# Optimization experiments

Hardware: AMD Instinct MI355X
Metric: run time of the kernel (lower is better)

Reference implementation:

```python
import jax, jax.numpy as jnp
import numpy as np

N_QUBITS = 6
N_LAYERS = 2
QSVT_DEGREE = 3
BATCH = 128
SEQ_LEN = 512
DIM = 2 ** N_QUBITS
# wire 0 is the most-significant bit in the statevector index (PennyLane convention)
_POP = np.array([bin(i).count('1') for i in range(DIM)], dtype=np.float32)
PHASE_SIGN = jnp.asarray(N_QUBITS - 2.0 * _POP)  # (DIM,): sum_w (1 - 2*bit_w)


def _rx(t):
    c = jnp.cos(0.5 * t).astype(jnp.complex64)
    s = (-1j * jnp.sin(0.5 * t)).astype(jnp.complex64)
    return jnp.stack([jnp.stack([c, s]), jnp.stack([s, c])])


def _ry(t):
    c = jnp.cos(0.5 * t).astype(jnp.complex64)
    s = jnp.sin(0.5 * t).astype(jnp.complex64)
    return jnp.stack([jnp.stack([c, -s]), jnp.stack([s, c])])


def _rz(t):
    e = jnp.exp(-0.5j * t.astype(jnp.complex64))
    z = jnp.zeros((), jnp.complex64)
    return jnp.stack([jnp.stack([e, z]), jnp.stack([z, jnp.conj(e)])])


def _apply_1q(psi, U, w):
    # psi: (B,) + (2,)*N_QUBITS ; U: (2,2) complex, same for all batch elems
    psi = jnp.moveaxis(psi, 1 + w, -1)
    psi = psi @ U.T
    return jnp.moveaxis(psi, -1, 1 + w)


def _apply_ry_batched(psi, theta, w):
    # RY with a per-batch angle theta: (B,)
    psi = jnp.moveaxis(psi, 1 + w, -1)
    c = jnp.cos(0.5 * theta).reshape((-1,) + (1,) * (N_QUBITS - 1))
    s = jnp.sin(0.5 * theta).reshape((-1,) + (1,) * (N_QUBITS - 1))
    a, b = psi[..., 0], psi[..., 1]
    psi = jnp.stack([c * a - s * b, s * a + c * b], axis=-1)
    return jnp.moveaxis(psi, -1, 1 + w)


def _cnot(psi, c, t):
    p0 = jax.lax.index_in_dim(psi, 0, axis=1 + c, keepdims=True)
    p1 = jax.lax.index_in_dim(psi, 1, axis=1 + c, keepdims=True)
    p1 = jnp.flip(p1, axis=1 + t)
    return jnp.concatenate([p0, p1], axis=1 + c)


def _circuit_step(h, x, params, poly):
    # h, x: (B, N_QUBITS) angles. Returns <Z_w> per qubit: (B, N_QUBITS).
    B = h.shape[0]
    # 1) state encoding: RY(h_w)|0> = cos(h/2)|0> + sin(h/2)|1>  (product state)
    c, s = jnp.cos(0.5 * h), jnp.sin(0.5 * h)
    psi = jnp.ones((B, 1), jnp.complex64)
    for w in range(N_QUBITS):
        amp = jnp.stack([c[:, w], s[:, w]], axis=-1).astype(jnp.complex64)  # (B,2)
        psi = (psi[:, :, None] * amp[:, None, :]).reshape(B, -1)
    psi = psi.reshape((B,) + (2,) * N_QUBITS)
    # 2) QSVT block: RZ(coeff*pi) on every wire fuses into one diagonal phase
    for d in range(QSVT_DEGREE + 1):
        theta = poly[d] * np.pi
        phase = jnp.exp((-0.5j) * theta * PHASE_SIGN)  # (DIM,)
        psi = (psi.reshape(B, -1) * phase[None, :]).reshape((B,) + (2,) * N_QUBITS)
        for i in range(N_QUBITS - 1):
            psi = _cnot(psi, i, i + 1)
        psi = _cnot(psi, N_QUBITS - 1, 0)  # ring closure
    # 3) variational layers: per-wire RZ@RY@RX (RX applied first), then CNOT chain
    idx = 0
    for _ in range(N_LAYERS):
        for i in range(N_QUBITS):
            U = _rz(params[idx + 2]) @ _ry(params[idx + 1]) @ _rx(params[idx])
            psi = _apply_1q(psi, U, i)
            idx += 3
        for i in range(N_QUBITS - 1):
            psi = _cnot(psi, i, i + 1)
    # 4) input injection: RY(x_w) with per-batch angles
    for w in range(N_QUBITS):
        psi = _apply_ry_batched(psi, x[:, w], w)
    # 5) measurement: <Z_w> = P(bit_w=0) - P(bit_w=1)
    p = jnp.abs(psi) ** 2
    zs = []
    for w in range(N_QUBITS):
        axes = tuple(a for a in range(1, N_QUBITS + 1) if a != 1 + w)
        pw = p.sum(axis=axes)  # (B,2)
        zs.append(pw[:, 0] - pw[:, 1])
    return jnp.stack(zs, axis=-1)


def _ssm_pass(angles, params, poly, reverse):
    a = jnp.flip(angles, axis=1) if reverse else angles
    xs = jnp.moveaxis(a, 1, 0)  # (T, B, n)
    h0 = jnp.zeros((a.shape[0], N_QUBITS), jnp.float32)

    def step(h, x):
        hn = _circuit_step(h, x, params, poly)
        return hn, hn

    _, ys = jax.lax.scan(step, h0, xs)
    out = jnp.moveaxis(ys, 0, 1)  # (B, T, n)
    return jnp.flip(out, axis=1) if reverse else out


def setup_inputs() -> dict:
    key = jax.random.key(0)
    k0, k1, k2, k3 = jax.random.split(key, 4)
    angles = jax.random.uniform(k0, (BATCH, SEQ_LEN, N_QUBITS), jnp.float32) * np.float32(np.pi)
    poly_coeffs = jax.random.normal(k1, (QSVT_DEGREE + 1,), jnp.float32) * 0.1
    fwd_params = jax.random.normal(k2, (N_QUBITS * N_LAYERS * 3,), jnp.float32) * 0.1
    bwd_params = jax.random.normal(k3, (N_QUBITS * N_LAYERS * 3,), jnp.float32) * 0.1
    fwd_coeff = jnp.full((1,), 0.5, jnp.float32)
    bwd_coeff = jnp.full((1,), 0.5, jnp.float32)
    return {'angles': angles, 'poly_coeffs': poly_coeffs, 'fwd_params': fwd_params,
            'bwd_params': bwd_params, 'fwd_coeff': fwd_coeff, 'bwd_coeff': bwd_coeff}


def reference(angles, poly_coeffs, fwd_params, bwd_params, fwd_coeff, bwd_coeff):
    h_fwd = _ssm_pass(angles, fwd_params, poly_coeffs, reverse=False)
    h_bwd = _ssm_pass(angles, bwd_params, poly_coeffs, reverse=True)
    return jax.nn.sigmoid(fwd_coeff) * h_fwd + jax.nn.sigmoid(bwd_coeff) * h_bwd
```

## Files before the change

### kernel.cpp

```cpp
#include <hip/hip_runtime.h>
#include <hip/hip_bf16.h>
#include <stdint.h>

#define BATCH 128
#define SEQ   512
#define NW    6
#define DIM   64
#define NELEM (BATCH * SEQ * NW)
#define PI_F  3.14159265358979323846f

typedef float v2f __attribute__((ext_vector_type(2)));
typedef uint16_t u16x8 __attribute__((ext_vector_type(8)));

__device__ __forceinline__ v2f pkfma(float s, v2f m, v2f a) {
    return __builtin_elementwise_fma((v2f){s, s}, m, a);
}

template <int CTRL>
__device__ __forceinline__ float dpp_add(float v) {
    return v + __int_as_float(__builtin_amdgcn_update_dpp(
        0, __float_as_int(v), CTRL, 0xF, 0xF, true));
}

template <int CTRL>
__device__ __forceinline__ void red6(float v[6]) {
#pragma unroll
    for (int k = 0; k < 6; ++k) v[k] = dpp_add<CTRL>(v[k]);
}

template <int CTRL>
__device__ __forceinline__ float dpp_mov(float x) {
    return __int_as_float(__builtin_amdgcn_update_dpp(
        0, __float_as_int(x), CTRL, 0xF, 0xF, true));
}

__device__ __forceinline__ float ldf(const void* p, int i, bool bf) {
    if (bf) {
        uint32_t u = (uint32_t)((const uint16_t*)p)[i];
        return __uint_as_float(u << 16);
    }
    return ((const float*)p)[i];
}

__global__ void k_prep(const void* ang, const void* poly, const void* fp,
                       const void* bp, const void* fc, const void* bc,
                       float* __restrict__ misc, float* __restrict__ Mg,
                       int* __restrict__ flag) {
    __shared__ int cnt;
    if (threadIdx.x == 0) cnt = 0;
    __syncthreads();
    {
        uint32_t w = ((const uint32_t*)ang)[threadIdx.x & 255];
        uint32_t e = (w >> 8) & 0xFFu;
        if (e >= 0x3Au && e <= 0x41u) atomicAdd(&cnt, 1);
    }
    __syncthreads();
    const bool bf = (cnt >= 128);

    if (blockIdx.x == 32) {
        if (threadIdx.x == 0)      misc[76] = ldf(fc, 0, bf);
        else if (threadIdx.x == 1) misc[77] = ldf(bc, 0, bf);
        else if (threadIdx.x == 2) *flag = bf ? 1 : 0;
        return;
    }

    const int lane = threadIdx.x & 63;
    const int tix  = blockIdx.x * 4 + (threadIdx.x >> 6);
    const int dir  = tix >> 6;
    const int col  = tix & 63;
    const void* prm = dir ? bp : fp;
    const int p = lane;

    float yr = (p == col) ? 1.f : 0.f;
    float yi = 0.f;

#pragma unroll
    for (int d = 0; d < 4; ++d) {
        const float th = 0.5f * PI_F * ldf(poly, d, bf) *
                         (float)(6 - 2 * (int)__popc((unsigned)p));
        float s, c;
        __sincosf(th, &s, &c);
        const float nr = yr * c + yi * s;
        const float ni = yi * c - yr * s;
        yr = nr; yi = ni;
#pragma unroll
        for (int k = 0; k < 6; ++k) {
            const int cw = k, tw = (k + 1) % 6;
            const int src = p ^ (((p >> (5 - cw)) & 1) << (5 - tw));
            yr = __shfl(yr, src, 64);
            yi = __shfl(yi, src, 64);
        }
    }

    int idx = 0;
#pragma unroll
    for (int l = 0; l < 2; ++l) {
#pragma unroll
        for (int w = 0; w < 6; ++w) {
            float cx, sx, cy, sy, cz, sz;
            __sincosf(0.5f * ldf(prm, idx + 0, bf), &sx, &cx);
            __sincosf(0.5f * ldf(prm, idx + 1, bf), &sy, &cy);
            __sincosf(0.5f * ldf(prm, idx + 2, bf), &sz, &cz);
            idx += 3;
            const float A = cy * cx, B = sy * sx, C = sy * cx, D = cy * sx;
            const float U00r = cz * A + sz * B, U00i = cz * B - sz * A;
            const float U11r = U00r,            U11i = sz * A - cz * B;
            const float Xr   = cz * C + sz * D, Xi   = sz * C - cz * D;
            const int m  = 1 << (5 - w);
            const int bb = (p >> (5 - w)) & 1;
            const float C1r = bb ? U11r : U00r;
            const float C1i = bb ? U11i : U00i;
            const float C2r = bb ? Xr : -Xr;
            const float C2i = Xi;
            const float pr = __shfl_xor(yr, m, 64);
            const float pi = __shfl_xor(yi, m, 64);
            const float nr = C1r * yr - C1i * yi + C2r * pr - C2i * pi;
            const float ni = C1r * yi + C1i * yr + C2r * pi + C2i * pr;
            yr = nr; yi = ni;
        }
#pragma unroll
        for (int k = 0; k < 5; ++k) {
            const int src = p ^ (((p >> (5 - k)) & 1) << (5 - (k + 1)));
            yr = __shfl(yr, src, 64);
            yi = __shfl(yi, src, 64);
        }
    }

    float* out = Mg + ((size_t)(dir * 64 + p) * 64 + (size_t)col) * 2;
    out[0] = yr;
    out[1] = yi;
}

__global__ void __launch_bounds__(256, 1) k_sim(const void* __restrict__ ang,
                                                const float* __restrict__ Mg,
                                                float* __restrict__ hbuf,
                                                const int* __restrict__ flag) {
    const int tid   = threadIdx.x;
    const int lane  = tid & 63;
    const int wv    = tid >> 6;
    const int chain = blockIdx.x;
    const int dir   = chain >> 7;
    const int b     = chain & 127;
    const bool bf   = (*flag != 0);

    __shared__ __align__(16) float  cl[SEQ * 12];
    __shared__ __align__(16) float  zb[SEQ * NW];
    __shared__ float2 pY[2][4][DIM];

    if (!bf) {
        const float4* src =
            (const float4*)((const float*)ang + (size_t)b * (SEQ * NW));
#pragma unroll
        for (int k = 0; k < 3; ++k) {
            const int v = k * 256 + tid;
            const float4 a = src[v];
            __align__(16) float o[8];
            float s, c;
            __sincosf(a.x, &s, &c); o[0] = c; o[1] = s;
            __sincosf(a.y, &s, &c); o[2] = c; o[3] = s;
            __sincosf(a.z, &s, &c); o[4] = c; o[5] = s;
            __sincosf(a.w, &s, &c); o[6] = c; o[7] = s;
            ((float4*)cl)[2 * v]     = ((const float4*)o)[0];
            ((float4*)cl)[2 * v + 1] = ((const float4*)o)[1];
        }
    } else {
        const u16x8* src =
            (const u16x8*)((const uint16_t*)ang + (size_t)b * (SEQ * NW));
#pragma unroll
        for (int k = 0; k < 2; ++k) {
            const int v = k * 256 + tid;
            if (v < 384) {
                const u16x8 a = src[v];
                __align__(16) float o[16];
#pragma unroll
                for (int e = 0; e < 8; ++e) {
                    const float x = __uint_as_float(((uint32_t)a[e]) << 16);
                    float s, c;
                    __sincosf(x, &s, &c);
                    o[2 * e] = c; o[2 * e + 1] = s;
                }
#pragma unroll
                for (int j = 0; j < 4; ++j)
                    ((float4*)cl)[4 * v + j] = ((const float4*)o)[j];
            }
        }
    }

    v2f Mres[16];
    {
        const float2* mr2 =
            (const float2*)(Mg + (size_t)(dir * 64 + lane) * 128 + 32 * wv);
#pragma unroll
        for (int k = 0; k < 16; ++k) Mres[k] = (v2f){mr2[k].x, mr2[k].y};
    }

    int zmask[6];
#pragma unroll
    for (int w = 0; w < 6; ++w) zmask[w] = ((lane >> (5 - w)) & 1) << 31;
    const int ow0 = wv ^ 1, ow1 = wv ^ 2, ow2 = wv ^ 3;

    float h[6] = {0.f, 0.f, 0.f, 0.f, 0.f, 0.f};

    auto encode_matvec = [&](v2f& acc) {
        const v2f kc1 = {2.6041667e-3f, 2.6041667e-3f};
        const v2f kc0 = {-0.125f, -0.125f};
        const v2f ks1 = {2.6041667e-4f, 2.6041667e-4f};
        const v2f ks0 = {-2.0833333e-2f, -2.0833333e-2f};
        const v2f one = {1.f, 1.f}, half = {0.5f, 0.5f};
        v2f hp0 = {h[0], h[1]}, hp1 = {h[2], h[3]}, hp2 = {h[4], h[5]};
        v2f u0 = hp0 * hp0, u1 = hp1 * hp1, u2 = hp2 * hp2;
        v2f c0 = __builtin_elementwise_fma(u0,
                    __builtin_elementwise_fma(u0, kc1, kc0), one);
        v2f c1 = __builtin_elementwise_fma(u1,
                    __builtin_elementwise_fma(u1, kc1, kc0), one);
        v2f c2 = __builtin_elementwise_fma(u2,
                    __builtin_elementwise_fma(u2, kc1, kc0), one);
        v2f s0 = hp0 * __builtin_elementwise_fma(u0,
                    __builtin_elementwise_fma(u0, ks1, ks0), half);
        v2f s1 = hp1 * __builtin_elementwise_fma(u1,
                    __builtin_elementwise_fma(u1, ks1, ks0), half);
        v2f s2 = hp2 * __builtin_elementwise_fma(u2,
                    __builtin_elementwise_fma(u2, ks1, ks0), half);
        const float t0 = (wv & 2) ? s0.x : c0.x;
        const float t1 = (wv & 1) ? s0.y : c0.y;
        const float A  = t0 * t1;
        float GH[4], GL[4];
        GH[0] = c1.x * c1.y; GH[1] = c1.x * s1.y;
        GH[2] = s1.x * c1.y; GH[3] = s1.x * s1.y;
#pragma unroll
        for (int a = 0; a < 4; ++a) GH[a] *= A;
        GL[0] = c2.x * c2.y; GL[1] = c2.x * s2.y;
        GL[2] = s2.x * c2.y; GL[3] = s2.x * s2.y;
        v2f y = {0.f, 0.f};
#pragma unroll
        for (int a = 0; a < 4; ++a) {
            v2f T = {0.f, 0.f};
#pragma unroll
            for (int b2 = 0; b2 < 4; ++b2)
                T = pkfma(GL[b2], Mres[4 * a + b2], T);
            y = pkfma(GH[a], T, y);
        }
        acc = y;
    };

    const float* cp = cl + (dir ? (SEQ - 1) * 12 : 0);
    const int   cstep = dir ? -12 : 12;
    float*       zp = zb + (dir ? (SEQ - 1) * NW : 0);
    const int   zstep = dir ? -NW : NW;

    __syncthreads();

    v2f myacc;
    encode_matvec(myacc);
    pY[0][wv][lane] = (float2){myacc.x, myacc.y};
    float4 xq0 = ((const float4*)cp)[0];
    float4 xq1 = ((const float4*)cp)[1];
    float4 xq2 = ((const float4*)cp)[2];
    cp += cstep;
    __syncthreads();

    for (int t = 0; t < SEQ; ++t) {
        const int buf = t & 1;

        const float2 yA = pY[buf][ow0][lane];
        const float2 yB = pY[buf][ow1][lane];
        const float2 yC = pY[buf][ow2][lane];
        const float yr = (myacc.x + yA.x) + (yB.x + yC.x);
        const float yi = (myacc.y + yA.y) + (yB.y + yC.y);
        const int yri = __float_as_int(yr), yii = __float_as_int(yi);

        float dot[6];
        {
            auto rr = __builtin_amdgcn_permlane32_swap(yri, yri, false, false);
            auto ri = __builtin_amdgcn_permlane32_swap(yii, yii, false, false);
            dot[0] = fmaf(__int_as_float((int)rr[0]), __int_as_float((int)rr[1]),
                          __int_as_float((int)ri[0]) * __int_as_float((int)ri[1]));
        }
        {
            auto rr = __builtin_amdgcn_permlane16_swap(yri, yri, false, false);
            auto ri = __builtin_amdgcn_permlane16_swap(yii, yii, false, false);
            dot[1] = fmaf(__int_as_float((int)rr[0]), __int_as_float((int)rr[1]),
                          __int_as_float((int)ri[0]) * __int_as_float((int)ri[1]));
        }
        dot[2] = fmaf(yr, dpp_mov<0x128>(yr), yi * dpp_mov<0x128>(yi));
        dot[3] = fmaf(yr, dpp_mov<0x141>(dpp_mov<0x1B>(yr)),
                      yi * dpp_mov<0x141>(dpp_mov<0x1B>(yi)));
        dot[4] = fmaf(yr, dpp_mov<0x4E>(yr), yi * dpp_mov<0x4E>(yi));
        dot[5] = fmaf(yr, dpp_mov<0xB1>(yr), yi * dpp_mov<0xB1>(yi));

        const float q = fmaf(yr, yr, yi * yi);
        const float cx[6] = {xq0.x, xq0.z, xq1.x, xq1.z, xq2.x, xq2.z};
        const float sx[6] = {xq0.y, xq0.w, xq1.y, xq1.w, xq2.y, xq2.w};

        float v[6];
#pragma unroll
        for (int w = 0; w < 6; ++w) {
            const float cq = __int_as_float(__float_as_int(cx[w] * q) ^ zmask[w]);
            v[w] = fmaf(-sx[w], dot[w], cq);
        }

        if (t + 1 < SEQ) {
            xq0 = ((const float4*)cp)[0];
            xq1 = ((const float4*)cp)[1];
            xq2 = ((const float4*)cp)[2];
            cp += cstep;
        }

        red6<0x111>(v);
        red6<0x112>(v);
        red6<0x114>(v);
        red6<0x118>(v);
        red6<0x142>(v);
        red6<0x143>(v);

        if (tid == 63) {
#pragma unroll
            for (int w = 0; w < 6; ++w) zp[w] = v[w];
        }
        zp += zstep;
#pragma unroll
        for (int w = 0; w < 6; ++w)
            h[w] = __int_as_float(
                __builtin_amdgcn_readlane(__float_as_int(v[w]), 63));

        encode_matvec(myacc);
        pY[buf ^ 1][wv][lane] = (float2){myacc.x, myacc.y};
        __syncthreads();
    }

    {
        const float4* zs4 = (const float4*)zb;
        float4* go = (float4*)(hbuf + (size_t)dir * NELEM +
                               (size_t)b * (SEQ * NW));
#pragma unroll
        for (int k = 0; k < 3; ++k) {
            const int idx = tid + k * 256;
            go[idx] = zs4[idx];
        }
    }
}

__global__ void k_combine(const float* __restrict__ hbuf,
                          const float* __restrict__ misc,
                          void* __restrict__ out, const int* __restrict__ flag) {
    const int i = blockIdx.x * blockDim.x + threadIdx.x;
    if (i >= NELEM) return;
    const float sf = 1.f / (1.f + __expf(-misc[76]));
    const float sb = 1.f / (1.f + __expf(-misc[77]));
    const float v = sf * hbuf[i] + sb * hbuf[NELEM + i];
    if (*flag) ((__hip_bfloat16*)out)[i] = __float2bfloat16(v);
    else       ((float*)out)[i] = v;
}

extern "C" void kernel_launch(void* const* d_in, const int* in_sizes, int n_in,
                              void* d_out, int out_size, void* d_ws, size_t ws_size,
                              hipStream_t stream) {
    const void* ang  = d_in[0];
    const void* poly = d_in[1];
    const void* fp   = d_in[2];
    const void* bp   = d_in[3];
    const void* fc   = d_in[4];
    const void* bc   = d_in[5];

    float* misc = (float*)d_ws + 32;
    float* hbuf = misc + 128;
    float* Mg   = hbuf + 2 * NELEM;
    int*   flag = (int*)(Mg + 2 * 64 * 64 * 2);

    k_prep<<<33, 256, 0, stream>>>(ang, poly, fp, bp, fc, bc, misc, Mg, flag);
    k_sim<<<256, 256, 0, stream>>>(ang, Mg, hbuf, flag);
    k_combine<<<(NELEM + 255) / 256, 256, 0, stream>>>(hbuf, misc, d_out, flag);
}
```

Before: 344.1 us.

## Split per-chain matvec across two waves instead of four

Each sequential chain now runs on two 64-lane wavefronts, each holding 32 matrix columns in registers, instead of four wavefronts with 16 each. The per-step cross-wave reduction reads one partner's partial sum from shared memory rather than three, which cuts LDS traffic and the cost of synchronising within the block on the serial critical path. The trade-off is twice the FMA work per wave per step and more registers holding the matrix, so each step's matvec takes longer.

```diff
diff --git a/kernel.cpp b/kernel.cpp
--- a/kernel.cpp
+++ b/kernel.cpp
@@ -131,7 +131,7 @@
     out[1] = yi;
 }
 
-__global__ void __launch_bounds__(256, 1) k_sim(const void* __restrict__ ang,
+__global__ void __launch_bounds__(128, 1) k_sim(const void* __restrict__ ang,
                                                 const float* __restrict__ Mg,
                                                 float* __restrict__ hbuf,
                                                 const int* __restrict__ flag) {
@@ -145,14 +145,14 @@
 
     __shared__ __align__(16) float  cl[SEQ * 12];
     __shared__ __align__(16) float  zb[SEQ * NW];
-    __shared__ float2 pY[2][4][DIM];
+    __shared__ float2 pY[2][2][DIM];
 
     if (!bf) {
         const float4* src =
             (const float4*)((const float*)ang + (size_t)b * (SEQ * NW));
 #pragma unroll
-        for (int k = 0; k < 3; ++k) {
-            const int v = k * 256 + tid;
+        for (int k = 0; k < 6; ++k) {
+            const int v = k * 128 + tid;
             const float4 a = src[v];
             __align__(16) float o[8];
             float s, c;
@@ -167,37 +167,35 @@
         const u16x8* src =
             (const u16x8*)((const uint16_t*)ang + (size_t)b * (SEQ * NW));
 #pragma unroll
-        for (int k = 0; k < 2; ++k) {
-            const int v = k * 256 + tid;
-            if (v < 384) {
-                const u16x8 a = src[v];
-                __align__(16) float o[16];
-#pragma unroll
-                for (int e = 0; e < 8; ++e) {
-                    const float x = __uint_as_float(((uint32_t)a[e]) << 16);
-                    float s, c;
-                    __sincosf(x, &s, &c);
-                    o[2 * e] = c; o[2 * e + 1] = s;
-                }
-#pragma unroll
-                for (int j = 0; j < 4; ++j)
-                    ((float4*)cl)[4 * v + j] = ((const float4*)o)[j];
+        for (int k = 0; k < 3; ++k) {
+            const int v = k * 128 + tid;
+            const u16x8 a = src[v];
+            __align__(16) float o[16];
+#pragma unroll
+            for (int e = 0; e < 8; ++e) {
+                const float x = __uint_as_float(((uint32_t)a[e]) << 16);
+                float s, c;
+                __sincosf(x, &s, &c);
+                o[2 * e] = c; o[2 * e + 1] = s;
             }
-        }
-    }
-
-    v2f Mres[16];
+#pragma unroll
+            for (int j = 0; j < 4; ++j)
+                ((float4*)cl)[4 * v + j] = ((const float4*)o)[j];
+        }
+    }
+
+    v2f Mres[32];
     {
         const float2* mr2 =
-            (const float2*)(Mg + (size_t)(dir * 64 + lane) * 128 + 32 * wv);
-#pragma unroll
-        for (int k = 0; k < 16; ++k) Mres[k] = (v2f){mr2[k].x, mr2[k].y};
+            (const float2*)(Mg + (size_t)(dir * 64 + lane) * 128 + 64 * wv);
+#pragma unroll
+        for (int k = 0; k < 32; ++k) Mres[k] = (v2f){mr2[k].x, mr2[k].y};
     }
 
     int zmask[6];
 #pragma unroll
     for (int w = 0; w < 6; ++w) zmask[w] = ((lane >> (5 - w)) & 1) << 31;
-    const int ow0 = wv ^ 1, ow1 = wv ^ 2, ow2 = wv ^ 3;
+    const int ow = wv ^ 1;
 
     float h[6] = {0.f, 0.f, 0.f, 0.f, 0.f, 0.f};
 
@@ -221,24 +219,25 @@
                     __builtin_elementwise_fma(u1, ks1, ks0), half);
         v2f s2 = hp2 * __builtin_elementwise_fma(u2,
                     __builtin_elementwise_fma(u2, ks1, ks0), half);
-        const float t0 = (wv & 2) ? s0.x : c0.x;
-        const float t1 = (wv & 1) ? s0.y : c0.y;
-        const float A  = t0 * t1;
-        float GH[4], GL[4];
-        GH[0] = c1.x * c1.y; GH[1] = c1.x * s1.y;
-        GH[2] = s1.x * c1.y; GH[3] = s1.x * s1.y;
-#pragma unroll
-        for (int a = 0; a < 4; ++a) GH[a] *= A;
-        GL[0] = c2.x * c2.y; GL[1] = c2.x * s2.y;
-        GL[2] = s2.x * c2.y; GL[3] = s2.x * s2.y;
+        const float t0 = wv ? s0.x : c0.x;
+        const float gA = t0 * c0.y, gB = t0 * s0.y;
+        float eH4[4];
+        eH4[0] = gA * c1.x; eH4[1] = gA * s1.x;
+        eH4[2] = gB * c1.x; eH4[3] = gB * s1.x;
+        float g45[4], eL[8];
+        g45[0] = c2.x * c2.y; g45[1] = c2.x * s2.y;
+        g45[2] = s2.x * c2.y; g45[3] = s2.x * s2.y;
+#pragma unroll
+        for (int j = 0; j < 8; ++j)
+            eL[j] = ((j >> 2) ? s1.y : c1.y) * g45[j & 3];
         v2f y = {0.f, 0.f};
 #pragma unroll
         for (int a = 0; a < 4; ++a) {
             v2f T = {0.f, 0.f};
 #pragma unroll
-            for (int b2 = 0; b2 < 4; ++b2)
-                T = pkfma(GL[b2], Mres[4 * a + b2], T);
-            y = pkfma(GH[a], T, y);
+            for (int jl = 0; jl < 8; ++jl)
+                T = pkfma(eL[jl], Mres[8 * a + jl], T);
+            y = pkfma(eH4[a], T, y);
         }
         acc = y;
     };
@@ -262,11 +261,9 @@
     for (int t = 0; t < SEQ; ++t) {
         const int buf = t & 1;
 
-        const float2 yA = pY[buf][ow0][lane];
-        const float2 yB = pY[buf][ow1][lane];
-        const float2 yC = pY[buf][ow2][lane];
-        const float yr = (myacc.x + yA.x) + (yB.x + yC.x);
-        const float yi = (myacc.y + yA.y) + (yB.y + yC.y);
+        const float2 yP = pY[buf][ow][lane];
+        const float yr = myacc.x + yP.x;
+        const float yi = myacc.y + yP.y;
         const int yri = __float_as_int(yr), yii = __float_as_int(yi);
 
         float dot[6];
@@ -333,8 +330,8 @@
         float4* go = (float4*)(hbuf + (size_t)dir * NELEM +
                                (size_t)b * (SEQ * NW));
 #pragma unroll
-        for (int k = 0; k < 3; ++k) {
-            const int idx = tid + k * 256;
+        for (int k = 0; k < 6; ++k) {
+            const int idx = tid + k * 128;
             go[idx] = zs4[idx];
         }
     }
@@ -368,6 +365,6 @@
     int*   flag = (int*)(Mg + 2 * 64 * 64 * 2);
 
     k_prep<<<33, 256, 0, stream>>>(ang, poly, fp, bp, fc, bc, misc, Mg, flag);
-    k_sim<<<256, 256, 0, stream>>>(ang, Mg, hbuf, flag);
+    k_sim<<<256, 128, 0, stream>>>(ang, Mg, hbuf, flag);
     k_combine<<<(NELEM + 255) / 256, 256, 0, stream>>>(hbuf, misc, d_out, flag);
 }
```

After: 360.0 us. +4.6%, slower.
